# Kernel tuning notes

Measured on AMD Instinct MI355X. Metric: run time of the kernel, lower is better.

Reference implementation:

```python
import jax, jax.numpy as jnp
import numpy as np

OUT_H, OUT_W = 7, 7
SPATIAL_SCALE = 0.125
SAMPLING_RATIO = 2


def setup_inputs() -> dict:
    key = jax.random.key(0)
    k1, k2, k3, k4 = jax.random.split(key, 4)
    inputs = jax.random.normal(k1, (2, 100, 100, 256), dtype=jnp.float32)
    # boxes in image coords (stride-8 feature over ~800px image): x0,y0,x1,y1
    xy0 = jax.random.uniform(k2, (1024, 2), minval=0.0, maxval=600.0)
    wh = jax.random.uniform(k3, (1024, 2), minval=8.0, maxval=200.0)
    boxes = jnp.concatenate([xy0, xy0 + wh], axis=1).astype(jnp.float32)
    box_inds = jax.random.randint(k4, (1024,), 0, 2, dtype=jnp.int32)
    return {"inputs": inputs, "boxes": boxes, "box_inds": box_inds}


def _roi_align(inputs, boxes, box_inds):
    """aligned=True ROIAlign: crop_and_resize at oversampled grid + avg pool.

    Sample coordinate (per aligned=True transform + tf.crop_and_resize):
      x_j = x0*scale + spacing_w*(j+0.5) - 0.5, spacing_w = w_box*scale/crop_w
    Out-of-range samples get extrapolation_value=0 (TF semantics).
    """
    N, H, W, C = inputs.shape
    B = boxes.shape[0]
    ch, cw = OUT_H * SAMPLING_RATIO, OUT_W * SAMPLING_RATIO

    sb = boxes * SPATIAL_SCALE
    x0, y0, x1, y1 = sb[:, 0], sb[:, 1], sb[:, 2], sb[:, 3]
    sw = (x1 - x0) / cw  # [B]
    sh = (y1 - y0) / ch
    xs = x0[:, None] + sw[:, None] * (jnp.arange(cw, dtype=sb.dtype) + 0.5) - 0.5  # [B,cw]
    ys = y0[:, None] + sh[:, None] * (jnp.arange(ch, dtype=sb.dtype) + 0.5) - 0.5  # [B,ch]

    yl = jnp.floor(ys)
    xl = jnp.floor(xs)
    ty = ys - yl  # [B,ch]
    tx = xs - xl  # [B,cw]
    yli = jnp.clip(yl, 0, H - 1).astype(jnp.int32)
    yhi = jnp.clip(yl + 1, 0, H - 1).astype(jnp.int32)
    xli = jnp.clip(xl, 0, W - 1).astype(jnp.int32)
    xhi = jnp.clip(xl + 1, 0, W - 1).astype(jnp.int32)

    b = box_inds[:, None, None]

    def g(yy, xx):  # gather -> [B,ch,cw,C]
        return inputs[b, yy[:, :, None], xx[:, None, :], :]

    txe = tx[:, None, :, None]
    top = g(yli, xli) * (1.0 - txe) + g(yli, xhi) * txe
    bot = g(yhi, xli) * (1.0 - txe) + g(yhi, xhi) * txe
    tye = ty[:, :, None, None]
    out = top * (1.0 - tye) + bot * tye  # [B,ch,cw,C]

    valid = ((ys >= 0) & (ys <= H - 1))[:, :, None] & ((xs >= 0) & (xs <= W - 1))[:, None, :]
    out = jnp.where(valid[..., None], out, 0.0)

    # avg_pool2d kernel=stride=SAMPLING_RATIO (SAME==VALID since exact multiple)
    out = out.reshape(B, OUT_H, SAMPLING_RATIO, OUT_W, SAMPLING_RATIO, C).mean(axis=(2, 4))
    return out  # [B, OUT_H, OUT_W, C]


def reference(inputs, boxes, box_inds):
    return _roi_align(inputs, boxes, box_inds)
```

## Files before the change

### kernel.cpp

```cpp
#include <hip/hip_runtime.h>


constexpr int   H_IN  = 100;
constexpr int   W_IN  = 100;
constexpr int   C_IN  = 256;
constexpr int   OUT_H = 7;
constexpr int   OUT_W = 7;
constexpr int   NPIX  = OUT_H * OUT_W;
constexpr int   NBOX  = 1024;
constexpr float SCALE = 0.125f;

typedef float f32x4 __attribute__((ext_vector_type(4)));

struct Meta { int4 off; float4 w; };

constexpr int RMETA_OFF = 4096;
constexpr int CMETA_OFF = 4096 + 7168 * 32;

__global__ __launch_bounds__(1024) void sort_boxes_kernel(
    const float* __restrict__ boxes,
    const int*   __restrict__ box_inds,
    int*         __restrict__ perm)
{
    const int tid  = threadIdx.x;
    const int wave = tid >> 6;
    const int lane = tid & 63;

    const float y0 = boxes[tid * 4 + 1] * SCALE;
    const float y1 = boxes[tid * 4 + 3] * SCALE;
    const float cy = 0.5f * (y0 + y1);
    int band = (int)(cy * (1.0f / 25.0f));
    band = min(max(band, 0), 3);
    const int bin = box_inds[tid] * 4 + band;

    __shared__ int whist[16][8];
    __shared__ int sc[129];

    int wrank = 0;
    const unsigned long long ltmask = (lane == 63) ? ~0ull >> 1
                                                   : (1ull << lane) - 1;
#pragma unroll
    for (int k = 0; k < 8; ++k) {
        const unsigned long long bal = __ballot(bin == k);
        if (bin == k) wrank = __popcll(bal & ltmask);
        if (lane == 0) whist[wave][k] = __popcll(bal);
    }
    __syncthreads();

    if (tid < 128) sc[tid + 1] = whist[tid & 15][tid >> 4];
    if (tid == 0)  sc[0] = 0;
    __syncthreads();
    for (int off = 1; off < 128; off <<= 1) {
        int v = 0;
        if (tid < 128 && tid >= off) v = sc[tid - off + 1];
        __syncthreads();
        if (tid < 128 && tid >= off) sc[tid + 1] += v;
        __syncthreads();
    }

    perm[sc[bin * 16 + wave] + wrank] = tid;
}

__device__ __forceinline__ void fold_dim(float s0, float step, int LIM,
                                         int& c0, int& n, float* w)
{
    float s[2] = { s0, s0 + step };
    int   fl[2]; float t[2]; bool val[2];
    int lo = 0x7fffffff, hi = -0x7fffffff;
#pragma unroll
    for (int k = 0; k < 2; ++k) {
        const float f = floorf(s[k]);
        fl[k]  = (int)f;
        t[k]   = s[k] - f;
        val[k] = (s[k] >= 0.0f && s[k] <= (float)(LIM - 1));
        if (val[k]) {
            lo = min(lo, fl[k]);
            hi = max(hi, min(fl[k] + 1, LIM - 1));
        }
    }
    w[0] = w[1] = w[2] = w[3] = 0.0f;
    if (lo > hi) {
        c0 = min(max(fl[0], 0), LIM - 1);
        n  = 1;
        return;
    }
    c0 = lo;
    n  = hi - lo + 1;
#pragma unroll
    for (int k = 0; k < 2; ++k) {
        if (val[k]) {
            w[fl[k] - lo]                    += 1.0f - t[k];
            w[min(fl[k] + 1, LIM - 1) - lo]  += t[k];
        }
    }
}

__global__ __launch_bounds__(256) void meta_kernel(
    const float* __restrict__ boxes,
    const int*   __restrict__ box_inds,
    const int*   __restrict__ perm,
    Meta*        __restrict__ rmeta,
    Meta*        __restrict__ cmeta)
{
    const int t = blockIdx.x * 256 + threadIdx.x;
    if (t >= NBOX * 14) return;
    const int slot = t / 14;
    const int d    = t - slot * 14;

    const int b = perm[slot];
    const int n = box_inds[b];

    const float bx0 = boxes[b * 4 + 0] * SCALE;
    const float by0 = boxes[b * 4 + 1] * SCALE;
    const float bx1 = boxes[b * 4 + 2] * SCALE;
    const float by1 = boxes[b * 4 + 3] * SCALE;
    const float sw  = (bx1 - bx0) * (1.0f / 14.0f);
    const float sh  = (by1 - by0) * (1.0f / 14.0f);

    int c0, cnt; float wgt[4];
    Meta m;
    m.off.y = m.off.z = m.off.w = 0;
    if (d < 7) {
        const float s0 = by0 + sh * ((float)(d * 2) + 0.5f) - 0.5f;
        fold_dim(s0, sh, H_IN, c0, cnt, wgt);
        m.off.x = (n * (H_IN * W_IN * C_IN) + c0 * (W_IN * C_IN)) | (cnt - 1);
        m.w.x = wgt[0] * 0.25f; m.w.y = wgt[1] * 0.25f;
        m.w.z = wgt[2] * 0.25f; m.w.w = wgt[3] * 0.25f;
        rmeta[slot * 7 + d] = m;
    } else {
        const int ox = d - 7;
        const float s0 = bx0 + sw * ((float)(ox * 2) + 0.5f) - 0.5f;
        fold_dim(s0, sw, W_IN, c0, cnt, wgt);
        m.off.x = (c0 << 3) | cnt;
        m.w.x = wgt[0]; m.w.y = wgt[1]; m.w.z = wgt[2]; m.w.w = wgt[3];
        cmeta[slot * 7 + ox] = m;
    }
}

template<int NR>
__device__ __forceinline__ void process_half(
    const float* __restrict__ inputs,
    const Meta*  __restrict__ cmeta,
    float*       __restrict__ out,
    int slotbase, int r0off, const float* wr,
    int b, int oy, int ox0, int npx, int c4)
{
    f32x4 ring[4][NR];
#pragma unroll
    for (int s = 0; s < 4; ++s)
#pragma unroll
        for (int r = 0; r < NR; ++r)
            ring[s][r] = f32x4{0.f, 0.f, 0.f, 0.f};

    int L = -1000000;

    for (int j = 0; j < npx; ++j) {
        const int ox = ox0 + j;
        const Meta cm = cmeta[slotbase + ox];
        const int pk = __builtin_amdgcn_readfirstlane(cm.off.x);
        const int c0 = pk >> 3;
        const int nc = pk & 7;
        const int lo = max(L, c0);
        const int hi = c0 + nc;

#pragma unroll
        for (int s = 0; s < 4; ++s) {
            const int cs = lo + ((s - lo) & 3);
            if (cs < hi) {
                const int cb = r0off + cs * C_IN + c4;
#pragma unroll
                for (int r = 0; r < NR; ++r)
                    ring[s][r] = *(const f32x4*)(inputs + cb + r * (W_IN * C_IN));
            }
        }
        L = hi > L ? hi : L;

        const float w0 = cm.w.x, w1 = cm.w.y, w2 = cm.w.z, w3 = cm.w.w;
        float ws0, ws1, ws2, ws3;
        switch (c0 & 3) {
            case 0:  ws0 = w0; ws1 = w1; ws2 = w2; ws3 = w3; break;
            case 1:  ws0 = w3; ws1 = w0; ws2 = w1; ws3 = w2; break;
            case 2:  ws0 = w2; ws1 = w3; ws2 = w0; ws3 = w1; break;
            default: ws0 = w1; ws1 = w2; ws2 = w3; ws3 = w0; break;
        }

        f32x4 acc = {0.f, 0.f, 0.f, 0.f};
#pragma unroll
        for (int r = 0; r < NR; ++r) {
            acc += ring[0][r] * (wr[r] * ws0);
            acc += ring[1][r] * (wr[r] * ws1);
            acc += ring[2][r] * (wr[r] * ws2);
            acc += ring[3][r] * (wr[r] * ws3);
        }

        float* op = out + ((size_t)b * NPIX + oy * OUT_W + ox) * C_IN + c4;
        __builtin_nontemporal_store(acc, (f32x4*)op);
    }
}

__global__ __launch_bounds__(256) void roi_align_kernel(
    const float* __restrict__ inputs,
    const int*   __restrict__ perm,
    const Meta*  __restrict__ rmeta,
    const Meta*  __restrict__ cmeta,
    float*       __restrict__ out)
{
    const int lane = threadIdx.x & 63;
    const int wv   = threadIdx.x >> 6;

    const int nchunk = gridDim.x >> 3;
    const int lbid   = (blockIdx.x & 7) * nchunk + (blockIdx.x >> 3);
    const int wgid   = lbid * 4 + wv;

    const int slot = wgid / 14;
    const int d    = wgid - slot * 14;
    const int oy   = d >> 1;
    const int half = d & 1;
    const int ox0  = half ? 4 : 0;
    const int npx  = half ? 3 : 4;

    const int b = __builtin_amdgcn_readfirstlane(perm[slot]);

    const Meta rm = rmeta[slot * 7 + oy];
    const int rpk   = __builtin_amdgcn_readfirstlane(rm.off.x);
    const int nrm1  = rpk & 3;
    const int r0off = rpk & ~3;
    const float wr[4] = { rm.w.x, rm.w.y, rm.w.z, rm.w.w };

    const int c4 = lane * 4;
    const int slotbase = slot * 7;

    switch (nrm1) {
        case 0:  process_half<1>(inputs, cmeta, out, slotbase, r0off, wr, b, oy, ox0, npx, c4); break;
        case 1:  process_half<2>(inputs, cmeta, out, slotbase, r0off, wr, b, oy, ox0, npx, c4); break;
        case 2:  process_half<3>(inputs, cmeta, out, slotbase, r0off, wr, b, oy, ox0, npx, c4); break;
        default: process_half<4>(inputs, cmeta, out, slotbase, r0off, wr, b, oy, ox0, npx, c4); break;
    }
}

extern "C" void kernel_launch(void* const* d_in, const int* in_sizes, int n_in,
                              void* d_out, int out_size, void* d_ws, size_t ws_size,
                              hipStream_t stream) {
    const float* inputs   = (const float*)d_in[0];
    const float* boxes    = (const float*)d_in[1];
    const int*   box_inds = (const int*)d_in[2];
    float*       out      = (float*)d_out;

    int*  perm  = (int*)d_ws;
    Meta* rmeta = (Meta*)((char*)d_ws + RMETA_OFF);
    Meta* cmeta = (Meta*)((char*)d_ws + CMETA_OFF);

    sort_boxes_kernel<<<1, NBOX, 0, stream>>>(boxes, box_inds, perm);
    meta_kernel<<<56, 256, 0, stream>>>(boxes, box_inds, perm, rmeta, cmeta);

    const int blocks = NBOX * 14 / 4;
    roi_align_kernel<<<blocks, 256, 0, stream>>>(inputs, perm, rmeta, cmeta, out);
}
```

Before: 34.10 us.

## Assign one output pixel per wavefront with precomputed per-pixel gather metadata

```diff
diff --git a/kernel.cpp b/kernel.cpp
--- a/kernel.cpp
+++ b/kernel.cpp
@@ -12,10 +12,7 @@
 
 typedef float f32x4 __attribute__((ext_vector_type(4)));
 
-struct Meta { int4 off; float4 w; };
-
-constexpr int RMETA_OFF = 4096;
-constexpr int CMETA_OFF = 4096 + 7168 * 32;
+constexpr int PMETA_OFF = 4096;
 
 __global__ __launch_bounds__(1024) void sort_boxes_kernel(
     const float* __restrict__ boxes,
@@ -95,17 +92,18 @@
     }
 }
 
-__global__ __launch_bounds__(256) void meta_kernel(
+__global__ __launch_bounds__(256) void pmeta_kernel(
     const float* __restrict__ boxes,
     const int*   __restrict__ box_inds,
     const int*   __restrict__ perm,
-    Meta*        __restrict__ rmeta,
-    Meta*        __restrict__ cmeta)
-{
-    const int t = blockIdx.x * 256 + threadIdx.x;
-    if (t >= NBOX * 14) return;
-    const int slot = t / 14;
-    const int d    = t - slot * 14;
+    int*         __restrict__ pm)
+{
+    const int p = blockIdx.x * 256 + threadIdx.x;
+    if (p >= NBOX * NPIX) return;
+    const int slot = p / NPIX;
+    const int rem  = p - slot * NPIX;
+    const int oy   = (rem * 37) >> 8;
+    const int ox   = rem - oy * 7;
 
     const int b = perm[slot];
     const int n = box_inds[b];
@@ -117,125 +115,90 @@
     const float sw  = (bx1 - bx0) * (1.0f / 14.0f);
     const float sh  = (by1 - by0) * (1.0f / 14.0f);
 
-    int c0, cnt; float wgt[4];
-    Meta m;
-    m.off.y = m.off.z = m.off.w = 0;
-    if (d < 7) {
-        const float s0 = by0 + sh * ((float)(d * 2) + 0.5f) - 0.5f;
-        fold_dim(s0, sh, H_IN, c0, cnt, wgt);
-        m.off.x = (n * (H_IN * W_IN * C_IN) + c0 * (W_IN * C_IN)) | (cnt - 1);
-        m.w.x = wgt[0] * 0.25f; m.w.y = wgt[1] * 0.25f;
-        m.w.z = wgt[2] * 0.25f; m.w.w = wgt[3] * 0.25f;
-        rmeta[slot * 7 + d] = m;
-    } else {
-        const int ox = d - 7;
-        const float s0 = bx0 + sw * ((float)(ox * 2) + 0.5f) - 0.5f;
-        fold_dim(s0, sw, W_IN, c0, cnt, wgt);
-        m.off.x = (c0 << 3) | cnt;
-        m.w.x = wgt[0]; m.w.y = wgt[1]; m.w.z = wgt[2]; m.w.w = wgt[3];
-        cmeta[slot * 7 + ox] = m;
-    }
-}
-
-template<int NR>
-__device__ __forceinline__ void process_half(
-    const float* __restrict__ inputs,
-    const Meta*  __restrict__ cmeta,
-    float*       __restrict__ out,
-    int slotbase, int r0off, const float* wr,
-    int b, int oy, int ox0, int npx, int c4)
-{
-    f32x4 ring[4][NR];
-#pragma unroll
-    for (int s = 0; s < 4; ++s)
-#pragma unroll
-        for (int r = 0; r < NR; ++r)
-            ring[s][r] = f32x4{0.f, 0.f, 0.f, 0.f};
-
-    int L = -1000000;
-
-    for (int j = 0; j < npx; ++j) {
-        const int ox = ox0 + j;
-        const Meta cm = cmeta[slotbase + ox];
-        const int pk = __builtin_amdgcn_readfirstlane(cm.off.x);
-        const int c0 = pk >> 3;
-        const int nc = pk & 7;
-        const int lo = max(L, c0);
-        const int hi = c0 + nc;
-
-#pragma unroll
-        for (int s = 0; s < 4; ++s) {
-            const int cs = lo + ((s - lo) & 3);
-            if (cs < hi) {
-                const int cb = r0off + cs * C_IN + c4;
-#pragma unroll
-                for (int r = 0; r < NR; ++r)
-                    ring[s][r] = *(const f32x4*)(inputs + cb + r * (W_IN * C_IN));
-            }
-        }
-        L = hi > L ? hi : L;
-
-        const float w0 = cm.w.x, w1 = cm.w.y, w2 = cm.w.z, w3 = cm.w.w;
-        float ws0, ws1, ws2, ws3;
-        switch (c0 & 3) {
-            case 0:  ws0 = w0; ws1 = w1; ws2 = w2; ws3 = w3; break;
-            case 1:  ws0 = w3; ws1 = w0; ws2 = w1; ws3 = w2; break;
-            case 2:  ws0 = w2; ws1 = w3; ws2 = w0; ws3 = w1; break;
-            default: ws0 = w1; ws1 = w2; ws2 = w3; ws3 = w0; break;
-        }
-
-        f32x4 acc = {0.f, 0.f, 0.f, 0.f};
-#pragma unroll
-        for (int r = 0; r < NR; ++r) {
-            acc += ring[0][r] * (wr[r] * ws0);
-            acc += ring[1][r] * (wr[r] * ws1);
-            acc += ring[2][r] * (wr[r] * ws2);
-            acc += ring[3][r] * (wr[r] * ws3);
-        }
-
-        float* op = out + ((size_t)b * NPIX + oy * OUT_W + ox) * C_IN + c4;
-        __builtin_nontemporal_store(acc, (f32x4*)op);
-    }
+    int r0, nr; float wr[4];
+    fold_dim(by0 + sh * ((float)(oy * 2) + 0.5f) - 0.5f, sh, H_IN, r0, nr, wr);
+    int c0, nc; float wc[4];
+    fold_dim(bx0 + sw * ((float)(ox * 2) + 0.5f) - 0.5f, sw, W_IN, c0, nc, wc);
+
+    int* q = pm + p * 12;
+    q[0] = n * (H_IN * W_IN * C_IN) + r0 * (W_IN * C_IN) + c0 * C_IN;
+    q[1] = (b * NPIX + rem) * C_IN;
+    q[2] = (nr - 1) * 4 + (nc - 1);
+    q[3] = 0;
+    float* qf = (float*)q;
+    qf[4] = wr[0] * 0.25f; qf[5] = wr[1] * 0.25f;
+    qf[6] = wr[2] * 0.25f; qf[7] = wr[3] * 0.25f;
+    qf[8] = wc[0]; qf[9] = wc[1]; qf[10] = wc[2]; qf[11] = wc[3];
+}
+
+template<int NR, int NC>
+__device__ __forceinline__ f32x4 gather(const float* __restrict__ src,
+                                        const float* wr, const float* wc)
+{
+    f32x4 v[NR][NC];
+#pragma unroll
+    for (int i = 0; i < NR; ++i)
+#pragma unroll
+        for (int j = 0; j < NC; ++j)
+            v[i][j] = *(const f32x4*)(src + i * (W_IN * C_IN) + j * C_IN);
+
+    f32x4 acc = {0.f, 0.f, 0.f, 0.f};
+#pragma unroll
+    for (int i = 0; i < NR; ++i)
+#pragma unroll
+        for (int j = 0; j < NC; ++j)
+            acc += v[i][j] * (wr[i] * wc[j]);
+    return acc;
 }
 
 __global__ __launch_bounds__(256) void roi_align_kernel(
     const float* __restrict__ inputs,
-    const int*   __restrict__ perm,
-    const Meta*  __restrict__ rmeta,
-    const Meta*  __restrict__ cmeta,
+    const int*   __restrict__ pm,
     float*       __restrict__ out)
 {
-    const int lane = threadIdx.x & 63;
-    const int wv   = threadIdx.x >> 6;
+    __shared__ int smeta[48];
+
+    const int tid  = threadIdx.x;
+    const int lane = tid & 63;
+    const int wv   = tid >> 6;
 
     const int nchunk = gridDim.x >> 3;
     const int lbid   = (blockIdx.x & 7) * nchunk + (blockIdx.x >> 3);
-    const int wgid   = lbid * 4 + wv;
-
-    const int slot = wgid / 14;
-    const int d    = wgid - slot * 14;
-    const int oy   = d >> 1;
-    const int half = d & 1;
-    const int ox0  = half ? 4 : 0;
-    const int npx  = half ? 3 : 4;
-
-    const int b = __builtin_amdgcn_readfirstlane(perm[slot]);
-
-    const Meta rm = rmeta[slot * 7 + oy];
-    const int rpk   = __builtin_amdgcn_readfirstlane(rm.off.x);
-    const int nrm1  = rpk & 3;
-    const int r0off = rpk & ~3;
-    const float wr[4] = { rm.w.x, rm.w.y, rm.w.z, rm.w.w };
-
-    const int c4 = lane * 4;
-    const int slotbase = slot * 7;
-
-    switch (nrm1) {
-        case 0:  process_half<1>(inputs, cmeta, out, slotbase, r0off, wr, b, oy, ox0, npx, c4); break;
-        case 1:  process_half<2>(inputs, cmeta, out, slotbase, r0off, wr, b, oy, ox0, npx, c4); break;
-        case 2:  process_half<3>(inputs, cmeta, out, slotbase, r0off, wr, b, oy, ox0, npx, c4); break;
-        default: process_half<4>(inputs, cmeta, out, slotbase, r0off, wr, b, oy, ox0, npx, c4); break;
-    }
+    const int p0     = lbid * 4;
+
+    if (tid < 48) smeta[tid] = pm[p0 * 12 + tid];
+    __syncthreads();
+
+    const int* m = smeta + wv * 12;
+    const int  base = m[0];
+    const int  oute = m[1];
+    const int  sel  = __builtin_amdgcn_readfirstlane(m[2]);
+    const float* wr = (const float*)(m + 4);
+    const float* wc = (const float*)(m + 8);
+
+    const float* src = inputs + base + lane * 4;
+
+    f32x4 acc;
+    switch (sel) {
+        case 0:  acc = gather<1, 1>(src, wr, wc); break;
+        case 1:  acc = gather<1, 2>(src, wr, wc); break;
+        case 2:  acc = gather<1, 3>(src, wr, wc); break;
+        case 3:  acc = gather<1, 4>(src, wr, wc); break;
+        case 4:  acc = gather<2, 1>(src, wr, wc); break;
+        case 5:  acc = gather<2, 2>(src, wr, wc); break;
+        case 6:  acc = gather<2, 3>(src, wr, wc); break;
+        case 7:  acc = gather<2, 4>(src, wr, wc); break;
+        case 8:  acc = gather<3, 1>(src, wr, wc); break;
+        case 9:  acc = gather<3, 2>(src, wr, wc); break;
+        case 10: acc = gather<3, 3>(src, wr, wc); break;
+        case 11: acc = gather<3, 4>(src, wr, wc); break;
+        case 12: acc = gather<4, 1>(src, wr, wc); break;
+        case 13: acc = gather<4, 2>(src, wr, wc); break;
+        case 14: acc = gather<4, 3>(src, wr, wc); break;
+        default: acc = gather<4, 4>(src, wr, wc); break;
+    }
+
+    __builtin_nontemporal_store(acc, (f32x4*)(out + oute + lane * 4));
 }
 
 extern "C" void kernel_launch(void* const* d_in, const int* in_sizes, int n_in,
@@ -246,13 +209,12 @@
     const int*   box_inds = (const int*)d_in[2];
     float*       out      = (float*)d_out;
 
-    int*  perm  = (int*)d_ws;
-    Meta* rmeta = (Meta*)((char*)d_ws + RMETA_OFF);
-    Meta* cmeta = (Meta*)((char*)d_ws + CMETA_OFF);
+    int* perm = (int*)d_ws;
+    int* pm   = (int*)((char*)d_ws + PMETA_OFF);
 
     sort_boxes_kernel<<<1, NBOX, 0, stream>>>(boxes, box_inds, perm);
-    meta_kernel<<<56, 256, 0, stream>>>(boxes, box_inds, perm, rmeta, cmeta);
-
-    const int blocks = NBOX * 14 / 4;
-    roi_align_kernel<<<blocks, 256, 0, stream>>>(inputs, perm, rmeta, cmeta, out);
-}
+    pmeta_kernel<<<196, 256, 0, stream>>>(boxes, box_inds, perm, pm);
+
+    const int blocks = NBOX * NPIX / 4;
+    roi_align_kernel<<<blocks, 256, 0, stream>>>(inputs, pm, out);
+}
```

Result: faster. 33.14 us (-2.8%).
